# Optimization experiments

Measured on AMD Instinct MI355X. Metric: run time of the kernel, lower is better.

Reference implementation:

```python
import jax, jax.numpy as jnp
import numpy as np

EPS = 0.01
N = 1 << 25  # 33,554,432 steps


def setup_inputs() -> dict:
    key = jax.random.key(0)
    # categories in 1..5 (cat==0 is a no-op skip in the original and would make
    # the output shape data-dependent, so we exclude it)
    annotation_series = jax.random.randint(key, (N,), 1, 6, dtype=jnp.int32)
    f = lambda v: jnp.full((1,), v, dtype=jnp.float32)
    return {
        "annotation_series": annotation_series,
        "origin_w": f(0.0),
        "big_decrease_w": f(-0.2),
        "decrease_w": f(-0.1),
        "same_w": f(0.0),
        "increase_w": f(0.1),
        "big_increase_w": f(0.2),
    }


def reference(annotation_series, origin_w, big_decrease_w, decrease_w, same_w,
              increase_w, big_increase_w):
    sg = jax.lax.stop_gradient  # clamp bounds come from .item() => detached in torch
    # Per-category change values (data-independent scalars), each shape (1,)
    c1 = jnp.minimum(big_decrease_w, sg(jnp.minimum(0.0, decrease_w)) - EPS)
    c2 = jnp.clip(decrease_w, sg(big_decrease_w) + EPS, 0.0 - EPS)
    c3 = jnp.clip(same_w, sg(decrease_w) + EPS, sg(increase_w) - EPS)
    c4 = jnp.clip(increase_w, 0.0 + EPS, sg(big_increase_w) - EPS)
    c5 = jnp.maximum(big_increase_w, sg(jnp.maximum(0.0, increase_w)) + EPS)
    changes = jnp.concatenate([c1, c2, c3, c4, c5])  # (5,)
    # gather per-step change, then prefix-sum: the fused form of the Python loop
    step = changes[annotation_series - 1]            # (N,)
    series = origin_w + jnp.cumsum(step)             # (N,)
    return jnp.concatenate([origin_w, series])       # (N+1,)
```

## Files before the change

kernel.cpp:

```cpp
#include <hip/hip_runtime.h>

#define EPSF 0.01f
#define THREADS 256
#define WAVES (THREADS / 64)
#define TILE (THREADS * 4)
#define TPB 16
#define CHUNK (TILE * TPB)

typedef unsigned long long u64;
typedef unsigned int u32;

__device__ __forceinline__ void load_changes(const float* bd, const float* de,
                                             const float* sa, const float* in,
                                             const float* bi, float ch[5]) {
    float vbd = *bd, vd = *de, vs = *sa, vi = *in, vbi = *bi;
    ch[0] = fminf(vbd, fminf(0.0f, vd) - EPSF);
    ch[1] = fminf(fmaxf(vd, vbd + EPSF), 0.0f - EPSF);
    ch[2] = fminf(fmaxf(vs, vd + EPSF), vi - EPSF);
    ch[3] = fminf(fmaxf(vi, 0.0f + EPSF), vbi - EPSF);
    ch[4] = fmaxf(vbi, fmaxf(0.0f, vi) + EPSF);
}

__device__ __forceinline__ float sel_change(int v, float c0, float c1, float c2,
                                            float c3, float c4) {
    return (v == 1) ? c0 : (v == 2) ? c1 : (v == 3) ? c2 : (v == 4) ? c3 : c4;
}

__global__ __launch_bounds__(THREADS) void k_count(const int* __restrict__ ann,
                                                   int* __restrict__ bcT,
                                                   long long n, int nb) {
    long long start = (long long)blockIdx.x * CHUNK;
    long long end = start + CHUNK;
    if (end > n) end = n;

    u64 pk = 0ull;
    for (long long i = start + (long long)threadIdx.x * 4; i < end;
         i += (long long)THREADS * 4) {
        if (i + 4 <= end) {
            int4 a = *reinterpret_cast<const int4*>(ann + i);
            pk += (1ull << ((a.x - 1) * 12)) + (1ull << ((a.y - 1) * 12)) +
                  (1ull << ((a.z - 1) * 12)) + (1ull << ((a.w - 1) * 12));
        } else {
            for (long long j = i; j < end; ++j)
                pk += (1ull << ((ann[j] - 1) * 12));
        }
    }

    int cnt[5];
#pragma unroll
    for (int c = 0; c < 5; ++c) cnt[c] = (int)((pk >> (c * 12)) & 0xFFFull);
    const int lane = threadIdx.x & 63, wv = threadIdx.x >> 6;
#pragma unroll
    for (int c = 0; c < 5; ++c) {
        int x = cnt[c];
#pragma unroll
        for (int off = 32; off > 0; off >>= 1) x += __shfl_down(x, off, 64);
        cnt[c] = x;
    }
    __shared__ int sred[WAVES][5];
    if (lane == 0) {
#pragma unroll
        for (int c = 0; c < 5; ++c) sred[wv][c] = cnt[c];
    }
    __syncthreads();
    if (threadIdx.x == 0) {
#pragma unroll
        for (int c = 0; c < 5; ++c)
            bcT[c * nb + blockIdx.x] =
                sred[0][c] + sred[1][c] + sred[2][c] + sred[3][c];
    }
}

__global__ __launch_bounds__(THREADS) void k_emit(
    const int* __restrict__ ann, const int* __restrict__ bcT,
    float* __restrict__ out, long long n, int nb, const float* org,
    const float* bd, const float* de, const float* sa, const float* in,
    const float* bi) {
    float ch[5];
    load_changes(bd, de, sa, in, bi, ch);
    const float c0 = ch[0], c1 = ch[1], c2 = ch[2], c3 = ch[3], c4 = ch[4];

    __shared__ int sred[WAVES][5];
    __shared__ float wsum[2][WAVES];
    __shared__ float s_base;

    const int tid = threadIdx.x, lane = tid & 63, wv = tid >> 6;
    const int vbid = blockIdx.x;

    int pc[5];
#pragma unroll
    for (int c = 0; c < 5; ++c) {
        int s = 0;
        for (int j = tid; j < vbid; j += THREADS) s += bcT[c * nb + j];
#pragma unroll
        for (int off = 32; off > 0; off >>= 1) s += __shfl_down(s, off, 64);
        pc[c] = s;
    }
    if (lane == 0) {
#pragma unroll
        for (int c = 0; c < 5; ++c) sred[wv][c] = pc[c];
    }
    __syncthreads();
    if (tid == 0) {
        double acc = (double)(*org);
#pragma unroll
        for (int c = 0; c < 5; ++c) {
            int tot = sred[0][c] + sred[1][c] + sred[2][c] + sred[3][c];
            acc += (double)tot * (double)ch[c];
        }
        s_base = (float)acc;
    }
    __syncthreads();

    const long long start = (long long)vbid * CHUNK;
    long long end = start + CHUNK;
    if (end > n) end = n;
    float running = s_base;

    for (int t = 0; t < TPB; ++t) {
        long long tb = start + (long long)t * TILE;
        if (tb >= end) break;
        long long i = tb + (long long)tid * 4;

        float e1, e2, e3, s;
        const bool vec = (i + 4 <= n);
        if (vec) {
            int4 a = *reinterpret_cast<const int4*>(ann + i);
            float d0 = sel_change(a.x, c0, c1, c2, c3, c4);
            float d1 = sel_change(a.y, c0, c1, c2, c3, c4);
            float d2 = sel_change(a.z, c0, c1, c2, c3, c4);
            float d3 = sel_change(a.w, c0, c1, c2, c3, c4);
            e1 = d0; e2 = e1 + d1; e3 = e2 + d2; s = e3 + d3;
        } else {
            float e[5];
            e[0] = 0.0f;
#pragma unroll
            for (int j = 0; j < 4; ++j) {
                float cv = 0.0f;
                if (i + j < n) cv = sel_change(ann[i + j], c0, c1, c2, c3, c4);
                e[j + 1] = e[j] + cv;
            }
            e1 = e[1]; e2 = e[2]; e3 = e[3]; s = e[4];
        }

        float x = s;
#pragma unroll
        for (int off = 1; off < 64; off <<= 1) {
            float y = __shfl_up(x, off, 64);
            if (lane >= off) x += y;
        }
        if (lane == 63) wsum[t & 1][wv] = x;
        __syncthreads();
        float w0 = wsum[t & 1][0], w1 = wsum[t & 1][1];
        float w2 = wsum[t & 1][2], w3 = wsum[t & 1][3];
        float waveOff = (wv > 0 ? w0 : 0.0f) + (wv > 1 ? w1 : 0.0f) +
                        (wv > 2 ? w2 : 0.0f);
        float total = w0 + w1 + w2 + w3;

        float b = running + waveOff + (x - s);
        if (vec) {
            *reinterpret_cast<float4*>(out + i) =
                make_float4(b, b + e1, b + e2, b + e3);
        } else {
            if (i + 0 < n) out[i + 0] = b;
            if (i + 1 < n) out[i + 1] = b + e1;
            if (i + 2 < n) out[i + 2] = b + e2;
            if (i + 3 < n) out[i + 3] = b + e3;
        }
        running += total;
    }
    if (end == n && start < n && tid == 0) out[n] = running;
}

extern "C" void kernel_launch(void* const* d_in, const int* in_sizes, int n_in,
                              void* d_out, int out_size, void* d_ws, size_t ws_size,
                              hipStream_t stream) {
    const int* ann = (const int*)d_in[0];
    const float* org = (const float*)d_in[1];
    const float* bd = (const float*)d_in[2];
    const float* de = (const float*)d_in[3];
    const float* sa = (const float*)d_in[4];
    const float* in = (const float*)d_in[5];
    const float* bi = (const float*)d_in[6];
    float* out = (float*)d_out;

    long long n = (long long)in_sizes[0];
    int nb = (int)((n + CHUNK - 1) / CHUNK);
    if (nb < 1) nb = 1;

    int* bcT = (int*)d_ws;

    k_count<<<nb, THREADS, 0, stream>>>(ann, bcT, n, nb);
    k_emit<<<nb, THREADS, 0, stream>>>(ann, bcT, out, n, nb, org, bd, de, sa,
                                       in, bi);
}
```

Measured before the change: 75.21 us.

## Fuse count and emit passes into one cooperative kernel with register-cached categories

Merges the count and emit kernels into one cooperative kernel that uses a grid-wide sync. Each thread packs its annotation categories into 4-bit nibbles held in registers, so the input is read from global memory only once instead of twice. Chunk size is doubled so the grid is 1024 blocks, few enough to be co-resident for the grid sync. This adds the risk that a cooperative launch fails if the blocks cannot all be resident, and it adds register pressure from the nibble array.

After: 163.0 us. 117% more time.

```diff
diff --git a/kernel.cpp b/kernel.cpp
--- a/kernel.cpp
+++ b/kernel.cpp
@@ -1,11 +1,15 @@
 #include <hip/hip_runtime.h>
+#include <hip/hip_cooperative_groups.h>
+
+namespace cg = cooperative_groups;
 
 #define EPSF 0.01f
 #define THREADS 256
 #define WAVES (THREADS / 64)
 #define TILE (THREADS * 4)
-#define TPB 16
+#define TPB 32
 #define CHUNK (TILE * TPB)
+#define NCW (TPB / 2)
 
 typedef unsigned long long u64;
 typedef unsigned int u32;
@@ -21,61 +25,15 @@
     ch[4] = fmaxf(vbi, fmaxf(0.0f, vi) + EPSF);
 }
 
-__device__ __forceinline__ float sel_change(int v, float c0, float c1, float c2,
-                                            float c3, float c4) {
-    return (v == 1) ? c0 : (v == 2) ? c1 : (v == 3) ? c2 : (v == 4) ? c3 : c4;
-}
-
-__global__ __launch_bounds__(THREADS) void k_count(const int* __restrict__ ann,
-                                                   int* __restrict__ bcT,
-                                                   long long n, int nb) {
-    long long start = (long long)blockIdx.x * CHUNK;
-    long long end = start + CHUNK;
-    if (end > n) end = n;
-
-    u64 pk = 0ull;
-    for (long long i = start + (long long)threadIdx.x * 4; i < end;
-         i += (long long)THREADS * 4) {
-        if (i + 4 <= end) {
-            int4 a = *reinterpret_cast<const int4*>(ann + i);
-            pk += (1ull << ((a.x - 1) * 12)) + (1ull << ((a.y - 1) * 12)) +
-                  (1ull << ((a.z - 1) * 12)) + (1ull << ((a.w - 1) * 12));
-        } else {
-            for (long long j = i; j < end; ++j)
-                pk += (1ull << ((ann[j] - 1) * 12));
-        }
-    }
-
-    int cnt[5];
-#pragma unroll
-    for (int c = 0; c < 5; ++c) cnt[c] = (int)((pk >> (c * 12)) & 0xFFFull);
-    const int lane = threadIdx.x & 63, wv = threadIdx.x >> 6;
-#pragma unroll
-    for (int c = 0; c < 5; ++c) {
-        int x = cnt[c];
-#pragma unroll
-        for (int off = 32; off > 0; off >>= 1) x += __shfl_down(x, off, 64);
-        cnt[c] = x;
-    }
-    __shared__ int sred[WAVES][5];
-    if (lane == 0) {
-#pragma unroll
-        for (int c = 0; c < 5; ++c) sred[wv][c] = cnt[c];
-    }
-    __syncthreads();
-    if (threadIdx.x == 0) {
-#pragma unroll
-        for (int c = 0; c < 5; ++c)
-            bcT[c * nb + blockIdx.x] =
-                sred[0][c] + sred[1][c] + sred[2][c] + sred[3][c];
-    }
-}
-
-__global__ __launch_bounds__(THREADS) void k_emit(
-    const int* __restrict__ ann, const int* __restrict__ bcT,
-    float* __restrict__ out, long long n, int nb, const float* org,
-    const float* bd, const float* de, const float* sa, const float* in,
-    const float* bi) {
+__device__ __forceinline__ float selc(u32 v, float c0, float c1, float c2,
+                                      float c3, float c4) {
+    return (v == 0) ? c0 : (v == 1) ? c1 : (v == 2) ? c2 : (v == 3) ? c3 : c4;
+}
+
+__global__ __launch_bounds__(THREADS, 4) void k_fused(
+    const int* __restrict__ ann, int* __restrict__ bcT, float* __restrict__ out,
+    long long n, int nb, const float* org, const float* bd, const float* de,
+    const float* sa, const float* in, const float* bi) {
     float ch[5];
     load_changes(bd, de, sa, in, bi, ch);
     const float c0 = ch[0], c1 = ch[1], c2 = ch[2], c3 = ch[3], c4 = ch[4];
@@ -86,6 +44,60 @@
 
     const int tid = threadIdx.x, lane = tid & 63, wv = tid >> 6;
     const int vbid = blockIdx.x;
+    const long long start = (long long)vbid * CHUNK;
+    long long end = start + CHUNK;
+    if (end > n) end = n;
+
+    u32 cw[NCW];
+#pragma unroll
+    for (int k = 0; k < NCW; ++k) cw[k] = 0;
+    u64 pk = 0ull;
+
+#pragma unroll
+    for (int t = 0; t < TPB; ++t) {
+        long long tb = start + (long long)t * TILE;
+        if (tb >= n) break;
+        long long i = tb + (long long)tid * 4;
+        u32 nib = 0;
+        if (i + 4 <= n) {
+            int4 a = *reinterpret_cast<const int4*>(ann + i);
+            u32 cx = (u32)(a.x - 1), cy = (u32)(a.y - 1);
+            u32 cz = (u32)(a.z - 1), cd = (u32)(a.w - 1);
+            pk += (1ull << (cx * 12)) + (1ull << (cy * 12)) +
+                  (1ull << (cz * 12)) + (1ull << (cd * 12));
+            nib = cx | (cy << 4) | (cz << 8) | (cd << 12);
+        } else {
+#pragma unroll
+            for (int j = 0; j < 4; ++j) {
+                if (i + j < n) {
+                    u32 c = (u32)(ann[i + j] - 1);
+                    pk += (1ull << (c * 12));
+                    nib |= c << (4 * j);
+                }
+            }
+        }
+        cw[t >> 1] |= nib << ((t & 1) * 16);
+    }
+
+    int cnt[5];
+#pragma unroll
+    for (int c = 0; c < 5; ++c) cnt[c] = (int)((pk >> (c * 12)) & 0xFFFull);
+#pragma unroll
+    for (int c = 0; c < 5; ++c) {
+        int s = cnt[c];
+#pragma unroll
+        for (int off = 32; off > 0; off >>= 1) s += __shfl_down(s, off, 64);
+        if (lane == 0) sred[wv][c] = s;
+    }
+    __syncthreads();
+    if (tid == 0) {
+#pragma unroll
+        for (int c = 0; c < 5; ++c)
+            bcT[c * nb + vbid] =
+                sred[0][c] + sred[1][c] + sred[2][c] + sred[3][c];
+    }
+
+    cg::this_grid().sync();
 
     int pc[5];
 #pragma unroll
@@ -96,6 +108,7 @@
         for (int off = 32; off > 0; off >>= 1) s += __shfl_down(s, off, 64);
         pc[c] = s;
     }
+    __syncthreads();
     if (lane == 0) {
 #pragma unroll
         for (int c = 0; c < 5; ++c) sred[wv][c] = pc[c];
@@ -112,36 +125,26 @@
     }
     __syncthreads();
 
-    const long long start = (long long)vbid * CHUNK;
-    long long end = start + CHUNK;
-    if (end > n) end = n;
     float running = s_base;
-
+#pragma unroll
     for (int t = 0; t < TPB; ++t) {
         long long tb = start + (long long)t * TILE;
         if (tb >= end) break;
         long long i = tb + (long long)tid * 4;
 
-        float e1, e2, e3, s;
+        u32 nib = cw[t >> 1] >> ((t & 1) * 16);
         const bool vec = (i + 4 <= n);
-        if (vec) {
-            int4 a = *reinterpret_cast<const int4*>(ann + i);
-            float d0 = sel_change(a.x, c0, c1, c2, c3, c4);
-            float d1 = sel_change(a.y, c0, c1, c2, c3, c4);
-            float d2 = sel_change(a.z, c0, c1, c2, c3, c4);
-            float d3 = sel_change(a.w, c0, c1, c2, c3, c4);
-            e1 = d0; e2 = e1 + d1; e3 = e2 + d2; s = e3 + d3;
-        } else {
-            float e[5];
-            e[0] = 0.0f;
-#pragma unroll
-            for (int j = 0; j < 4; ++j) {
-                float cv = 0.0f;
-                if (i + j < n) cv = sel_change(ann[i + j], c0, c1, c2, c3, c4);
-                e[j + 1] = e[j] + cv;
-            }
-            e1 = e[1]; e2 = e[2]; e3 = e[3]; s = e[4];
-        }
+        float d0 = selc(nib & 0xF, c0, c1, c2, c3, c4);
+        float d1 = selc((nib >> 4) & 0xF, c0, c1, c2, c3, c4);
+        float d2 = selc((nib >> 8) & 0xF, c0, c1, c2, c3, c4);
+        float d3 = selc((nib >> 12) & 0xF, c0, c1, c2, c3, c4);
+        if (!vec) {
+            if (i + 0 >= n) d0 = 0.0f;
+            if (i + 1 >= n) d1 = 0.0f;
+            if (i + 2 >= n) d2 = 0.0f;
+            if (i + 3 >= n) d3 = 0.0f;
+        }
+        float e1 = d0, e2 = e1 + d1, e3 = e2 + d2, s = e3 + d3;
 
         float x = s;
 #pragma unroll
@@ -190,7 +193,9 @@
 
     int* bcT = (int*)d_ws;
 
-    k_count<<<nb, THREADS, 0, stream>>>(ann, bcT, n, nb);
-    k_emit<<<nb, THREADS, 0, stream>>>(ann, bcT, out, n, nb, org, bd, de, sa,
-                                       in, bi);
-}
+    void* args[] = {(void*)&ann, (void*)&bcT, (void*)&out, (void*)&n,
+                    (void*)&nb,  (void*)&org, (void*)&bd,  (void*)&de,
+                    (void*)&sa,  (void*)&in,  (void*)&bi};
+    hipLaunchCooperativeKernel((const void*)k_fused, dim3(nb), dim3(THREADS),
+                               args, 0, stream);
+}
```
